# Optimization experiments

Measured on AMD Instinct MI355X. Metric: run time of the kernel, lower is better.

Reference implementation:

```python
import jax, jax.numpy as jnp
import numpy as np

B, T, IN, H, OUT = 64, 512, 256, 512, 256


def setup_inputs() -> dict:
    key = jax.random.key(0)
    ks = jax.random.split(key, 12)
    s_in = 1.0 / np.sqrt(H)  # PyTorch RNN init scale (uniform +-1/sqrt(H))
    u = lambda k, shape: jax.random.uniform(k, shape, jnp.float32, -s_in, s_in)
    return {
        "x": jax.random.normal(ks[0], (B, T, IN), jnp.float32),
        "W_ih0": u(ks[1], (H, IN)),
        "W_hh0": u(ks[2], (H, H)),
        "b_ih0": u(ks[3], (H,)),
        "b_hh0": u(ks[4], (H,)),
        "W_ih1": u(ks[5], (H, H)),
        "W_hh1": u(ks[6], (H, H)),
        "b_ih1": u(ks[7], (H,)),
        "b_hh1": u(ks[8], (H,)),
        "W_out": u(ks[9], (OUT, H)),
        "b_out": u(ks[10], (OUT,)),
    }


def _rnn_layer(seq, W_ih, W_hh, b_ih, b_hh):
    # seq: [B, T, D_in] -> outputs [B, T, H], last hidden [B, H]
    # Precompute input projection for all steps (one big GEMM).
    xp = jnp.einsum('btd,hd->bth', seq, W_ih) + b_ih + b_hh  # [B, T, H]
    xp_t = jnp.swapaxes(xp, 0, 1)  # [T, B, H] for scan over time
    h0 = jnp.zeros((seq.shape[0], W_hh.shape[0]), seq.dtype)

    def step(h, xpt):
        h = jnp.tanh(xpt + h @ W_hh.T)
        return h, h

    h_last, hs = jax.lax.scan(step, h0, xp_t)
    return jnp.swapaxes(hs, 0, 1), h_last


def reference(x, W_ih0, W_hh0, b_ih0, b_hh0, W_ih1, W_hh1, b_ih1, b_hh1, W_out, b_out):
    out0, _ = _rnn_layer(x, W_ih0, W_hh0, b_ih0, b_hh0)
    _, h_last = _rnn_layer(out0, W_ih1, W_hh1, b_ih1, b_hh1)
    return h_last @ W_out.T + b_out  # [B, OUT]
```

## Files before the change

### kernel.cpp

```cpp
#include <hip/hip_runtime.h>
#include <cmath>

#define B_   64
#define T_   512
#define IN_  256
#define H_   512
#define OUT_ 256
#define M_   (B_*T_)

typedef __bf16 bf16x4 __attribute__((ext_vector_type(4)));
typedef __bf16 bf16x8 __attribute__((ext_vector_type(8)));
typedef float  f32x4  __attribute__((ext_vector_type(4)));
typedef unsigned long long u64;

static __device__ __forceinline__ void split_f32(float x, __bf16 &hi, __bf16 &lo) {
    unsigned u  = __float_as_uint(x);
    unsigned hu = u & 0xffff0000u;
    hi = __builtin_bit_cast(__bf16, (unsigned short)(hu >> 16));
    lo = (__bf16)(x - __uint_as_float(hu));
}

__global__ void split_arr(const float* __restrict__ src, __bf16* __restrict__ hi,
                          __bf16* __restrict__ lo, int n) {
    int i = blockIdx.x * 256 + threadIdx.x;
    if (i < n) { __bf16 h, l; split_f32(src[i], h, l); hi[i] = h; lo[i] = l; }
}

__global__ void bias_comb(const float* __restrict__ a, const float* __restrict__ b,
                          float* __restrict__ o, int n) {
    int i = blockIdx.x * 256 + threadIdx.x;
    if (i < n) o[i] = a[i] + b[i];
}

#define GBM 128
#define GBN 64
#define GBK 32
#define LDA 40

__global__ __launch_bounds__(256) void gemm_xp(
    const float* __restrict__ A, const __bf16* __restrict__ Whi,
    const __bf16* __restrict__ Wlo, const float* __restrict__ bias,
    float* __restrict__ C, int K)
{
    __shared__ __bf16 sAhi[GBM*LDA], sAlo[GBM*LDA], sBhi[GBN*LDA], sBlo[GBN*LDA];
    const int tid = threadIdx.x;
    const int m0 = blockIdx.y * GBM, n0 = blockIdx.x * GBN;
    const int wave = tid >> 6, lane = tid & 63, lm = lane & 15, q = lane >> 4;

    f32x4 acc[2][4];
#pragma unroll
    for (int i = 0; i < 2; ++i)
#pragma unroll
        for (int j = 0; j < 4; ++j) acc[i][j] = (f32x4){0.f,0.f,0.f,0.f};

    for (int k0 = 0; k0 < K; k0 += GBK) {
        __syncthreads();
#pragma unroll
        for (int i = 0; i < 4; ++i) {
            int c = tid + i * 256;
            int row = c >> 3, pos = c & 7;
            float4 v = *(const float4*)(&A[(size_t)(m0+row)*K + k0 + pos*4]);
            __bf16 h0,l0,h1,l1,h2,l2,h3,l3;
            split_f32(v.x,h0,l0); split_f32(v.y,h1,l1);
            split_f32(v.z,h2,l2); split_f32(v.w,h3,l3);
            *(bf16x4*)(&sAhi[row*LDA + pos*4]) = (bf16x4){h0,h1,h2,h3};
            *(bf16x4*)(&sAlo[row*LDA + pos*4]) = (bf16x4){l0,l1,l2,l3};
        }
        {
            int row = tid >> 2, pos = (tid & 3) * 8;
            *(bf16x8*)(&sBhi[row*LDA + pos]) =
                *(const bf16x8*)(&Whi[(size_t)(n0+row)*K + k0 + pos]);
            *(bf16x8*)(&sBlo[row*LDA + pos]) =
                *(const bf16x8*)(&Wlo[(size_t)(n0+row)*K + k0 + pos]);
        }
        __syncthreads();

        bf16x8 ah[2], al[2], bh[4], bl[4];
#pragma unroll
        for (int mt = 0; mt < 2; ++mt) {
            int r = wave*32 + mt*16 + lm;
            ah[mt] = *(const bf16x8*)(&sAhi[r*LDA + q*8]);
            al[mt] = *(const bf16x8*)(&sAlo[r*LDA + q*8]);
        }
#pragma unroll
        for (int nt = 0; nt < 4; ++nt) {
            int r = nt*16 + lm;
            bh[nt] = *(const bf16x8*)(&sBhi[r*LDA + q*8]);
            bl[nt] = *(const bf16x8*)(&sBlo[r*LDA + q*8]);
        }
#pragma unroll
        for (int mt = 0; mt < 2; ++mt)
#pragma unroll
            for (int nt = 0; nt < 4; ++nt) {
                acc[mt][nt] = __builtin_amdgcn_mfma_f32_16x16x32_bf16(ah[mt], bh[nt], acc[mt][nt], 0,0,0);
                acc[mt][nt] = __builtin_amdgcn_mfma_f32_16x16x32_bf16(ah[mt], bl[nt], acc[mt][nt], 0,0,0);
                acc[mt][nt] = __builtin_amdgcn_mfma_f32_16x16x32_bf16(al[mt], bh[nt], acc[mt][nt], 0,0,0);
            }
    }
#pragma unroll
    for (int mt = 0; mt < 2; ++mt)
#pragma unroll
        for (int nt = 0; nt < 4; ++nt)
#pragma unroll
            for (int r = 0; r < 4; ++r) {
                int m = m0 + wave*32 + mt*16 + q*4 + r;
                int n = n0 + nt*16 + lm;
                C[(size_t)m*H_ + n] = acc[mt][nt][r] + bias[n];
            }
}

#define RLDA 528
#define RDEP 8
#define BH   (B_*H_)

#define KEEPALIVE(WH, WL) do { \
    _Pragma("unroll") \
    for (int kt = 0; kt < 16; ++kt) asm volatile("" : "+v"(WH[kt]), "+v"(WL[kt])); \
    } while (0)

#define MMA16(ACC, WH, WL) do { \
    _Pragma("unroll") \
    for (int kt = 0; kt < 16; ++kt) { \
        bf16x8 ah = *(const bf16x8*)(&sAhi[lm*RLDA + kt*32 + q*8]); \
        bf16x8 al = *(const bf16x8*)(&sAlo[lm*RLDA + kt*32 + q*8]); \
        ACC = __builtin_amdgcn_mfma_f32_16x16x32_bf16(ah, WH[kt], ACC, 0,0,0); \
        ACC = __builtin_amdgcn_mfma_f32_16x16x32_bf16(ah, WL[kt], ACC, 0,0,0); \
        ACC = __builtin_amdgcn_mfma_f32_16x16x32_bf16(al, WH[kt], ACC, 0,0,0); \
    } } while (0)

__global__ __launch_bounds__(256, 1) void rnn_fused(
    const float* __restrict__ xp0,
    const __bf16* __restrict__ w0hi, const __bf16* __restrict__ w0lo,
    const __bf16* __restrict__ wphi, const __bf16* __restrict__ wplo,
    const __bf16* __restrict__ w1hi, const __bf16* __restrict__ w1lo,
    const float* __restrict__ bias1,
    unsigned* __restrict__ h0ring,
    u64*      __restrict__ xp1ring,
    unsigned* __restrict__ h1ring,
    float* __restrict__ hlast,
    int* __restrict__ flags)
{
    __shared__ __bf16 sAhi[16*RLDA], sAlo[16*RLDA];
    const int tid  = threadIdx.x;
    const int role = blockIdx.x >> 5;
    const int sub  = blockIdx.x & 31;
    const int g    = sub >> 3;
    const int c    = sub & 7;
    const int m0g  = g * 16;
    const int n0   = c * 64;
    const int wave = tid >> 6, lane = tid & 63, lm = lane & 15, q = lane >> 4;
    const int ncol = n0 + wave*16 + lm;
    const int srow = tid >> 4, sseg = tid & 15;

    int* const f0 = flags + (0*4 + g)*32;
    int* const fP = flags + (1*4 + g)*32;
    int* const f1 = flags + (2*4 + g)*32;
    int* const f1c = f1 + c*4;

    const __bf16* Wh = (role == 0) ? w0hi : (role == 1) ? wphi : w1hi;
    const __bf16* Wl = (role == 0) ? w0lo : (role == 1) ? wplo : w1lo;
    bf16x8 wh[16], wl[16];
#pragma unroll
    for (int kt = 0; kt < 16; ++kt) {
        wh[kt] = *(const bf16x8*)(&Wh[(size_t)ncol*H_ + kt*32 + q*8]);
        wl[kt] = *(const bf16x8*)(&Wl[(size_t)ncol*H_ + kt*32 + q*8]);
    }

    auto stage = [&](const unsigned* base) {
        const u64* row = (const u64*)(base + (size_t)(m0g + srow)*H_);
        __bf16* dh = &sAhi[srow*RLDA];
        __bf16* dl = &sAlo[srow*RLDA];
        u64 vv[16];
#pragma unroll
        for (int j = 0; j < 16; ++j)
            vv[j] = __hip_atomic_load(&row[sseg + j*16], __ATOMIC_RELAXED,
                                      __HIP_MEMORY_SCOPE_AGENT);
#pragma unroll
        for (int j = 0; j < 16; ++j) {
            unsigned pa = (unsigned)vv[j], pb = (unsigned)(vv[j] >> 32);
            int c0 = (sseg + j*16) * 2;
            *(unsigned*)(dh + c0) = (pa >> 16) | (pb & 0xffff0000u);
            *(unsigned*)(dl + c0) = (pa & 0xffffu) | (pb << 16);
        }
    };
    auto poll32 = [&](int* f, int tv) {
        for (;;) {
            int v = __hip_atomic_load(&f[lane & 31], __ATOMIC_RELAXED,
                                      __HIP_MEMORY_SCOPE_AGENT);
            if (__all(v >= tv)) break;
            __builtin_amdgcn_s_sleep(1);
        }
    };
    auto poll4 = [&](int* f, int tv) {
        for (;;) {
            int v = __hip_atomic_load(&f[lane & 3], __ATOMIC_RELAXED,
                                      __HIP_MEMORY_SCOPE_AGENT);
            if (__all(v >= tv)) break;
            __builtin_amdgcn_s_sleep(1);
        }
    };
    auto signal = [&](int* fw, int tv) {
        asm volatile("s_waitcnt vmcnt(0)" ::: "memory");
        if (lane == 0)
            __hip_atomic_store(fw, tv, __ATOMIC_RELAXED, __HIP_MEMORY_SCOPE_AGENT);
    };

    if (role == 0) {
        int* const myf = f0 + c*4 + wave;
        for (int t = 0; t < T_; ++t) {
            KEEPALIVE(wh, wl);
            float xr[4];
#pragma unroll
            for (int r = 0; r < 4; ++r)
                xr[r] = xp0[((size_t)(m0g + q*4 + r)*T_ + t)*H_ + ncol];
            int bp = 0;
            if (t >= 8) bp = __hip_atomic_load(&fP[lane & 31], __ATOMIC_RELAXED,
                                               __HIP_MEMORY_SCOPE_AGENT);
            if (t) poll32(f0, t);
            __syncthreads();
            stage(h0ring + (size_t)(t & 7)*BH);
            __syncthreads();

            f32x4 acc = (f32x4){0.f,0.f,0.f,0.f};
            MMA16(acc, wh, wl);
            unsigned pk[4];
#pragma unroll
            for (int r = 0; r < 4; ++r) {
                float hv = tanhf(xr[r] + acc[r]);
                __bf16 hh, hl; split_f32(hv, hh, hl);
                pk[r] = ((unsigned)__builtin_bit_cast(unsigned short, hh) << 16)
                      |  (unsigned)__builtin_bit_cast(unsigned short, hl);
            }
            if (t >= 8 && !__all(bp >= t-7)) poll32(fP, t-7);
            unsigned* dst = h0ring + (size_t)((t+1) & 7)*BH;
#pragma unroll
            for (int r = 0; r < 4; ++r)
                __hip_atomic_store(&dst[(size_t)(m0g + q*4 + r)*H_ + ncol], pk[r],
                                   __ATOMIC_RELAXED, __HIP_MEMORY_SCOPE_AGENT);
            signal(myf, t+1);
        }
    } else if (role == 1) {
        int* const myf = fP + c*4 + wave;
        const float b1 = bias1[ncol];
        for (int t = 0; t < T_; ++t) {
            KEEPALIVE(wh, wl);
            int bp = 0;
            if (t >= 8) bp = __hip_atomic_load(&f1c[lane & 3], __ATOMIC_RELAXED,
                                               __HIP_MEMORY_SCOPE_AGENT);
            poll32(f0, t+1);
            __syncthreads();
            stage(h0ring + (size_t)((t+1) & 7)*BH);
            signal(myf, t+1);
            __syncthreads();

            f32x4 a2 = (f32x4){0.f,0.f,0.f,0.f};
            MMA16(a2, wh, wl);
            if (t >= 8 && !__all(bp >= t-7)) poll4(f1c, t-7);
            u64* dst = xp1ring + (size_t)(t & 7)*BH;
#pragma unroll
            for (int r = 0; r < 4; ++r) {
                u64 pv = ((u64)(unsigned)(t+1) << 32) | __float_as_uint(a2[r] + b1);
                __hip_atomic_store(&dst[(size_t)(m0g + q*4 + r)*H_ + ncol], pv,
                                   __ATOMIC_RELAXED, __HIP_MEMORY_SCOPE_AGENT);
            }
        }
    } else {
        int* const myf = f1 + c*4 + wave;
        for (int t = 0; t < T_; ++t) {
            KEEPALIVE(wh, wl);
            const u64* xs = xp1ring + (size_t)(t & 7)*BH;
            u64 xv[4];
#pragma unroll
            for (int r = 0; r < 4; ++r)
                xv[r] = __hip_atomic_load(&xs[(size_t)(m0g + q*4 + r)*H_ + ncol],
                                          __ATOMIC_RELAXED, __HIP_MEMORY_SCOPE_AGENT);
            if (t) poll32(f1, t);
            __syncthreads();
            stage(h1ring + (size_t)(t & 1)*BH);
            __syncthreads();

            f32x4 acc = (f32x4){0.f,0.f,0.f,0.f};
            MMA16(acc, wh, wl);
#pragma unroll
            for (int r = 0; r < 4; ++r) {
                while ((unsigned)(xv[r] >> 32) != (unsigned)(t+1)) {
                    __builtin_amdgcn_s_sleep(1);
                    xv[r] = __hip_atomic_load(&xs[(size_t)(m0g + q*4 + r)*H_ + ncol],
                                              __ATOMIC_RELAXED, __HIP_MEMORY_SCOPE_AGENT);
                }
            }
            unsigned* dst = h1ring + (size_t)((t+1) & 1)*BH;
#pragma unroll
            for (int r = 0; r < 4; ++r) {
                int m = m0g + q*4 + r;
                float hv = tanhf(__uint_as_float((unsigned)xv[r]) + acc[r]);
                __bf16 hh, hl; split_f32(hv, hh, hl);
                unsigned pkv = ((unsigned)__builtin_bit_cast(unsigned short, hh) << 16)
                             |  (unsigned)__builtin_bit_cast(unsigned short, hl);
                __hip_atomic_store(&dst[(size_t)m*H_ + ncol], pkv,
                                   __ATOMIC_RELAXED, __HIP_MEMORY_SCOPE_AGENT);
                if (t == T_-1) hlast[(size_t)m*H_ + ncol] = hv;
            }
            signal(myf, t+1);
        }
    }
}

__global__ __launch_bounds__(256) void out_proj(
    const float* __restrict__ hlast, const float* __restrict__ Wout,
    const float* __restrict__ bout, float* __restrict__ out)
{
    __shared__ float sh[H_];
    int b = blockIdx.x;
    for (int i = threadIdx.x; i < H_; i += 256) sh[i] = hlast[(size_t)b*H_ + i];
    __syncthreads();
    int o = threadIdx.x;
    const float* wr = &Wout[(size_t)o*H_];
    float acc = 0.f;
#pragma unroll 4
    for (int k = 0; k < H_; k += 4) {
        float4 wv = *(const float4*)(&wr[k]);
        acc += wv.x*sh[k] + wv.y*sh[k+1] + wv.z*sh[k+2] + wv.w*sh[k+3];
    }
    out[(size_t)b*OUT_ + o] = bout[o] + acc;
}

extern "C" void kernel_launch(void* const* d_in, const int* in_sizes, int n_in,
                              void* d_out, int out_size, void* d_ws, size_t ws_size,
                              hipStream_t stream)
{
    const float* x    = (const float*)d_in[0];
    const float* Wih0 = (const float*)d_in[1];
    const float* Whh0 = (const float*)d_in[2];
    const float* bih0 = (const float*)d_in[3];
    const float* bhh0 = (const float*)d_in[4];
    const float* Wih1 = (const float*)d_in[5];
    const float* Whh1 = (const float*)d_in[6];
    const float* bih1 = (const float*)d_in[7];
    const float* bhh1 = (const float*)d_in[8];
    const float* Wout = (const float*)d_in[9];
    const float* bout = (const float*)d_in[10];

    char* w = (char*)d_ws;
    size_t off = 0;
    auto alloc = [&](size_t bytes) -> void* {
        void* p = w + off; off = (off + bytes + 255) & ~(size_t)255; return p;
    };
    float*  xp     = (float*) alloc((size_t)M_*H_*4);
    __bf16* wih0hi = (__bf16*)alloc((size_t)H_*IN_*2);
    __bf16* wih0lo = (__bf16*)alloc((size_t)H_*IN_*2);
    __bf16* whh0hi = (__bf16*)alloc((size_t)H_*H_*2);
    __bf16* whh0lo = (__bf16*)alloc((size_t)H_*H_*2);
    __bf16* wih1hi = (__bf16*)alloc((size_t)H_*H_*2);
    __bf16* wih1lo = (__bf16*)alloc((size_t)H_*H_*2);
    __bf16* whh1hi = (__bf16*)alloc((size_t)H_*H_*2);
    __bf16* whh1lo = (__bf16*)alloc((size_t)H_*H_*2);
    float*  bias0  = (float*) alloc(H_*4);
    float*  bias1  = (float*) alloc(H_*4);
    size_t zstart = off;
    unsigned* h0ring = (unsigned*)alloc((size_t)RDEP*B_*H_*4);
    u64*      xp1ring= (u64*)     alloc((size_t)RDEP*B_*H_*8);
    unsigned* h1ring = (unsigned*)alloc((size_t)2*B_*H_*4);
    int*      flags  = (int*)     alloc(1536);
    size_t zlen = off - zstart;
    float*  hlast  = (float*) alloc((size_t)B_*H_*4);

    hipMemsetAsync(w + zstart, 0, zlen, stream);

    split_arr<<<(H_*IN_+255)/256, 256, 0, stream>>>(Wih0, wih0hi, wih0lo, H_*IN_);
    split_arr<<<(H_*H_ +255)/256, 256, 0, stream>>>(Whh0, whh0hi, whh0lo, H_*H_);
    split_arr<<<(H_*H_ +255)/256, 256, 0, stream>>>(Wih1, wih1hi, wih1lo, H_*H_);
    split_arr<<<(H_*H_ +255)/256, 256, 0, stream>>>(Whh1, whh1hi, whh1lo, H_*H_);
    bias_comb<<<2, 256, 0, stream>>>(bih0, bhh0, bias0, H_);
    bias_comb<<<2, 256, 0, stream>>>(bih1, bhh1, bias1, H_);

    dim3 ggrid(H_/GBN, M_/GBM);
    gemm_xp<<<ggrid, 256, 0, stream>>>(x, wih0hi, wih0lo, bias0, xp, IN_);

    rnn_fused<<<96, 256, 0, stream>>>(xp, whh0hi, whh0lo, wih1hi, wih1lo,
                                      whh1hi, whh1lo, bias1,
                                      h0ring, xp1ring, h1ring, hlast, flags);

    out_proj<<<B_, 256, 0, stream>>>(hlast, Wout, bout, (float*)d_out);
}
```

Measured before the change: 2.413 ms.

## Merge layer-1 input-projection role into layer-0 recurrence blocks

Removes the separate role of blocks that projected layer-0 hidden states through W_ih1. The layer-0 recurrence blocks now also hold W_ih1 in registers and, one step later, project the h0 tile they already staged into shared memory. This removes one extra staging of h0 per step, the fP flag handshake and 32 blocks, so the grid drops from 96 to 64. In exchange each layer-0 block does twice the MMA work per step and uses many more registers, which may lengthen the layer-0 critical path.

```diff
diff --git a/kernel.cpp b/kernel.cpp
--- a/kernel.cpp
+++ b/kernel.cpp
@@ -152,18 +152,25 @@
     const int ncol = n0 + wave*16 + lm;
     const int srow = tid >> 4, sseg = tid & 15;
 
-    int* const f0 = flags + (0*4 + g)*32;
-    int* const fP = flags + (1*4 + g)*32;
-    int* const f1 = flags + (2*4 + g)*32;
+    int* const f0  = flags + (0*4 + g)*32;
+    int* const f1  = flags + (1*4 + g)*32;
     int* const f1c = f1 + c*4;
 
-    const __bf16* Wh = (role == 0) ? w0hi : (role == 1) ? wphi : w1hi;
-    const __bf16* Wl = (role == 0) ? w0lo : (role == 1) ? wplo : w1lo;
+    const __bf16* Wh = role ? w1hi : w0hi;
+    const __bf16* Wl = role ? w1lo : w0lo;
     bf16x8 wh[16], wl[16];
 #pragma unroll
     for (int kt = 0; kt < 16; ++kt) {
         wh[kt] = *(const bf16x8*)(&Wh[(size_t)ncol*H_ + kt*32 + q*8]);
         wl[kt] = *(const bf16x8*)(&Wl[(size_t)ncol*H_ + kt*32 + q*8]);
+    }
+    bf16x8 ph[16], pl[16];
+    if (role == 0) {
+#pragma unroll
+        for (int kt = 0; kt < 16; ++kt) {
+            ph[kt] = *(const bf16x8*)(&wphi[(size_t)ncol*H_ + kt*32 + q*8]);
+            pl[kt] = *(const bf16x8*)(&wplo[(size_t)ncol*H_ + kt*32 + q*8]);
+        }
     }
 
     auto stage = [&](const unsigned* base) {
@@ -207,61 +214,54 @@
 
     if (role == 0) {
         int* const myf = f0 + c*4 + wave;
-        for (int t = 0; t < T_; ++t) {
+        const float b1 = bias1[ncol];
+        for (int t = 0; t <= T_; ++t) {
             KEEPALIVE(wh, wl);
+            KEEPALIVE(ph, pl);
             float xr[4];
-#pragma unroll
-            for (int r = 0; r < 4; ++r)
-                xr[r] = xp0[((size_t)(m0g + q*4 + r)*T_ + t)*H_ + ncol];
+            if (t < T_) {
+#pragma unroll
+                for (int r = 0; r < 4; ++r)
+                    xr[r] = xp0[((size_t)(m0g + q*4 + r)*T_ + t)*H_ + ncol];
+            }
             int bp = 0;
-            if (t >= 8) bp = __hip_atomic_load(&fP[lane & 31], __ATOMIC_RELAXED,
+            if (t >= 9) bp = __hip_atomic_load(&f1c[lane & 3], __ATOMIC_RELAXED,
                                                __HIP_MEMORY_SCOPE_AGENT);
             if (t) poll32(f0, t);
             __syncthreads();
             stage(h0ring + (size_t)(t & 7)*BH);
             __syncthreads();
 
-            f32x4 acc = (f32x4){0.f,0.f,0.f,0.f};
-            MMA16(acc, wh, wl);
-            unsigned pk[4];
-#pragma unroll
-            for (int r = 0; r < 4; ++r) {
-                float hv = tanhf(xr[r] + acc[r]);
-                __bf16 hh, hl; split_f32(hv, hh, hl);
-                pk[r] = ((unsigned)__builtin_bit_cast(unsigned short, hh) << 16)
-                      |  (unsigned)__builtin_bit_cast(unsigned short, hl);
-            }
-            if (t >= 8 && !__all(bp >= t-7)) poll32(fP, t-7);
-            unsigned* dst = h0ring + (size_t)((t+1) & 7)*BH;
-#pragma unroll
-            for (int r = 0; r < 4; ++r)
-                __hip_atomic_store(&dst[(size_t)(m0g + q*4 + r)*H_ + ncol], pk[r],
-                                   __ATOMIC_RELAXED, __HIP_MEMORY_SCOPE_AGENT);
-            signal(myf, t+1);
-        }
-    } else if (role == 1) {
-        int* const myf = fP + c*4 + wave;
-        const float b1 = bias1[ncol];
-        for (int t = 0; t < T_; ++t) {
-            KEEPALIVE(wh, wl);
-            int bp = 0;
-            if (t >= 8) bp = __hip_atomic_load(&f1c[lane & 3], __ATOMIC_RELAXED,
-                                               __HIP_MEMORY_SCOPE_AGENT);
-            poll32(f0, t+1);
-            __syncthreads();
-            stage(h0ring + (size_t)((t+1) & 7)*BH);
-            signal(myf, t+1);
-            __syncthreads();
-
-            f32x4 a2 = (f32x4){0.f,0.f,0.f,0.f};
-            MMA16(a2, wh, wl);
-            if (t >= 8 && !__all(bp >= t-7)) poll4(f1c, t-7);
-            u64* dst = xp1ring + (size_t)(t & 7)*BH;
-#pragma unroll
-            for (int r = 0; r < 4; ++r) {
-                u64 pv = ((u64)(unsigned)(t+1) << 32) | __float_as_uint(a2[r] + b1);
-                __hip_atomic_store(&dst[(size_t)(m0g + q*4 + r)*H_ + ncol], pv,
-                                   __ATOMIC_RELAXED, __HIP_MEMORY_SCOPE_AGENT);
+            if (t < T_) {
+                f32x4 acc = (f32x4){0.f,0.f,0.f,0.f};
+                MMA16(acc, wh, wl);
+                unsigned pk[4];
+#pragma unroll
+                for (int r = 0; r < 4; ++r) {
+                    float hv = tanhf(xr[r] + acc[r]);
+                    __bf16 hh, hl; split_f32(hv, hh, hl);
+                    pk[r] = ((unsigned)__builtin_bit_cast(unsigned short, hh) << 16)
+                          |  (unsigned)__builtin_bit_cast(unsigned short, hl);
+                }
+                unsigned* dst = h0ring + (size_t)((t+1) & 7)*BH;
+#pragma unroll
+                for (int r = 0; r < 4; ++r)
+                    __hip_atomic_store(&dst[(size_t)(m0g + q*4 + r)*H_ + ncol], pk[r],
+                                       __ATOMIC_RELAXED, __HIP_MEMORY_SCOPE_AGENT);
+                signal(myf, t+1);
+            }
+
+            if (t >= 1) {
+                f32x4 a2 = (f32x4){0.f,0.f,0.f,0.f};
+                MMA16(a2, ph, pl);
+                if (t >= 9 && !__all(bp >= t-8)) poll4(f1c, t-8);
+                u64* xdst = xp1ring + (size_t)((t-1) & 7)*BH;
+#pragma unroll
+                for (int r = 0; r < 4; ++r) {
+                    u64 pv = ((u64)(unsigned)t << 32) | __float_as_uint(a2[r] + b1);
+                    __hip_atomic_store(&xdst[(size_t)(m0g + q*4 + r)*H_ + ncol], pv,
+                                       __ATOMIC_RELAXED, __HIP_MEMORY_SCOPE_AGENT);
+                }
             }
         }
     } else {
@@ -361,7 +361,7 @@
     unsigned* h0ring = (unsigned*)alloc((size_t)RDEP*B_*H_*4);
     u64*      xp1ring= (u64*)     alloc((size_t)RDEP*B_*H_*8);
     unsigned* h1ring = (unsigned*)alloc((size_t)2*B_*H_*4);
-    int*      flags  = (int*)     alloc(1536);
+    int*      flags  = (int*)     alloc(1024);
     size_t zlen = off - zstart;
     float*  hlast  = (float*) alloc((size_t)B_*H_*4);
 
@@ -377,7 +377,7 @@
     dim3 ggrid(H_/GBN, M_/GBM);
     gemm_xp<<<ggrid, 256, 0, stream>>>(x, wih0hi, wih0lo, bias0, xp, IN_);
 
-    rnn_fused<<<96, 256, 0, stream>>>(xp, whh0hi, whh0lo, wih1hi, wih1lo,
+    rnn_fused<<<64, 256, 0, stream>>>(xp, whh0hi, whh0lo, wih1hi, wih1lo,
                                       whh1hi, whh1lo, bias1,
                                       h0ring, xp1ring, h1ring, hlast, flags);
 
```

After: 2.391 ms. Within noise of the previous version (-0.9%).
